# Performance work log

Measured on AMD Instinct MI355X. Metric: run time of the kernel, lower is better.

Reference implementation:

```python
import jax, jax.numpy as jnp
import numpy as np

SMOOTH = 1.0      # self.smooth
NUM_ITER = 10     # iter_
EPS = 1e-07
INF = 1e12        # stand-in for +inf in squared-distance init


def _maxpool(x, window):
    # torch max_pool3d(stride=1, padding=w//2): pad with -inf, window max
    pads = ((0, 0), (0, 0)) + tuple((w // 2, w // 2) for w in window)
    return jax.lax.reduce_window(x, -jnp.inf, jax.lax.max, (1, 1) + window, (1, 1, 1, 1, 1), pads)


def _soft_erode(x):  # x: [B,1,D,H,W]
    p1 = -_maxpool(-x, (3, 1, 1))
    p2 = -_maxpool(-x, (1, 3, 1))
    p3 = -_maxpool(-x, (1, 1, 3))
    return jnp.minimum(jnp.minimum(p1, p2), p3)


def _soft_open(x):
    return _maxpool(_soft_erode(x), (3, 3, 3))  # dilate(erode(x))


def _soft_skel(x, n_iter):
    skel = jax.nn.relu(x - _soft_open(x))
    for _ in range(n_iter):
        x = _soft_erode(x)
        delta = jax.nn.relu(x - _soft_open(x))
        skel = skel + jax.nn.relu(delta - skel * delta)
    return skel


def _edt_pass(d2, axis):
    # 1D squared-distance min-convolution: out[i] = min_j (i-j)^2 + d2[j]
    L = d2.shape[axis]
    d2m = jnp.moveaxis(d2, axis, -1)                 # [..., L]
    i = jnp.arange(L, dtype=d2.dtype)
    sq = (i[:, None] - i[None, :]) ** 2              # [L, L]
    out = jnp.min(d2m[..., None, :] + sq, axis=-1)   # [..., L]
    return jnp.moveaxis(out, -1, axis)


def _edt(mask):
    # exact Euclidean distance transform: distance of nonzero voxels to nearest zero voxel
    d2 = jnp.where(mask > 0, INF, 0.0).astype(jnp.float32)  # [B,D,H,W]
    for ax in (1, 2, 3):
        d2 = _edt_pass(d2, ax)
    return jnp.sqrt(d2)


def _get_weights(mask, skel):
    # mask, skel: [B,D,H,W] binary float
    dist = _edt(mask)
    dist = jnp.where(mask == 0, 0.0, dist)
    on_skel = skel == 1
    skel_r = jnp.where(on_skel, dist, 0.0)
    rmax = jnp.max(skel_r.reshape(skel_r.shape[0], -1), axis=1).reshape(-1, 1, 1, 1)
    valid = rmax > 0
    rmax_safe = jnp.where(valid, rmax, 1.0)
    dist_n = jnp.where(valid, dist / rmax_safe, dist)
    skel_rn = jnp.where(valid, skel_r / rmax_safe, skel_r)
    # dim == 3 branch: skel_1_R2_norm
    skel_1r2 = jnp.where(on_skel, (1.0 + EPS) / (skel_rn ** 2 + EPS), 0.0)
    return dist_n, skel_rn, skel_1r2


def _combine(A, B, C):
    # D = B*C, overwritten by A*C where (A != 0) & (B == 0)
    return jnp.where((A != 0) & (B == 0), A * C, B * C)


def reference(y_pred, y_true):
    # y_pred: [B,C,D,H,W] logits; y_true: [B,1,D,H,W] int labels
    fore = jnp.max(y_pred[:, 1:], axis=1, keepdims=True)
    logits = jnp.concatenate([y_pred[:, :1], fore], axis=1)   # [B,2,D,H,W]
    prob = jax.nn.softmax(logits, axis=1)
    yp = (prob[:, 1] > 0.5).astype(jnp.float32)               # [B,D,H,W]
    yt = (y_true > 0).astype(jnp.float32)[:, 0]               # [B,D,H,W]

    skel_p = _soft_skel(yp[:, None], NUM_ITER)[:, 0]
    skel_t = _soft_skel(yt[:, None], NUM_ITER)[:, 0]

    q_vl, q_slvl, q_sl = _get_weights(yt, skel_t)
    q_vp, q_spvp, q_sp = _get_weights(yp, skel_p)

    w_tprec = (jnp.sum(q_sp * q_vl) + SMOOTH) / (jnp.sum(_combine(q_spvp, q_slvl, q_sp)) + SMOOTH)
    w_tsens = (jnp.sum(q_sl * q_vp) + SMOOTH) / (jnp.sum(_combine(q_slvl, q_spvp, q_sl)) + SMOOTH)
    return 1.0 - 2.0 * (w_tprec * w_tsens) / (w_tprec + w_tsens)


def setup_inputs() -> dict:
    key = jax.random.key(0)
    k1, k2 = jax.random.split(key)
    y_pred = jax.random.normal(k1, (2, 2, 64, 96, 96), dtype=jnp.float32)
    y_true = jax.random.randint(k2, (2, 1, 64, 96, 96), 0, 2, dtype=jnp.int32)
    return {"y_pred": y_pred, "y_true": y_true}
```

## Files before the change

kernel.cpp:

```cpp
#include <hip/hip_runtime.h>

namespace {

constexpr int Bn = 2;
constexpr int Dn = 64;
constexpr int Hn = 96;
constexpr int Wn = 96;
constexpr int HW = Hn * Wn;
constexpr int S  = Dn * HW;
constexpr int NBS = Bn * S;
constexpr int NT  = 2 * NBS;
constexpr int WPR = Wn / 32;
constexpr int WPP = HW / 32;
constexpr int WPS = S / 32;
constexpr int NTW = NT / 32;
constexpr float EPSf = 1e-7f;
constexpr int BLK_SUMS = NBS / 4 / 256;
#define BIGF 1e12f

__global__ __launch_bounds__(256) void k_bin_edt0(const float* __restrict__ logits,
                                                  const int* __restrict__ labels,
                                                  unsigned* __restrict__ Mb,
                                                  float* __restrict__ D2) {
  __shared__ unsigned bits[64];
  __shared__ unsigned zlo[32], zhi[32];
  int slab = blockIdx.x / 288;
  int cg = blockIdx.x - slab * 288;
  int c0 = cg * 32;
  int tid = threadIdx.x;
  int lane = tid & 63;
  for (int t = tid; t < 2048; t += 256) {
    int zz = t >> 5;
    int col = t & 31;
    int s = zz * HW + c0 + col;
    bool v;
    if (slab < 2) {
      float l0 = logits[(slab * 2 + 0) * S + s];
      float l1 = logits[(slab * 2 + 1) * S + s];
      v = l1 > l0;
    } else {
      v = labels[(slab - 2) * S + s] > 0;
    }
    unsigned long long m = __ballot(v);
    if (lane == 0) {
      unsigned w = (unsigned)m;
      bits[zz] = w;
      Mb[slab * WPS + zz * WPP + cg] = w;
    } else if (lane == 32) {
      unsigned w = (unsigned)(m >> 32);
      bits[zz] = w;
      Mb[slab * WPS + zz * WPP + cg] = w;
    }
  }
  __syncthreads();
  if (tid < 64) {
    int col = tid & 31;
    int base = (tid < 32) ? 0 : 32;
    unsigned zw = 0u;
    #pragma unroll
    for (int j = 0; j < 32; ++j)
      zw |= (((bits[base + j] >> col) & 1u) ^ 1u) << j;
    if (tid < 32) zlo[col] = zw; else zhi[col] = zw;
  }
  __syncthreads();
  int col = tid & 31;
  int chunk = tid >> 5;
  int i0 = chunk * 8;
  unsigned long long Z = ((unsigned long long)zhi[col] << 32) | (unsigned long long)zlo[col];
  float* o = D2 + slab * S + c0 + col;
  #pragma unroll
  for (int s = 0; s < 8; ++s) {
    int i = i0 + s;
    unsigned long long below = Z & ((2ull << i) - 1ull);
    unsigned long long above = Z >> i;
    float outv;
    if (below | above) {
      int ddn = below ? (i - (63 - __builtin_clzll(below))) : 99;
      int dup = above ? __builtin_ctzll(above) : 99;
      int d = ddn < dup ? ddn : dup;
      outv = (float)(d * d);
    } else {
      outv = BIGF;
    }
    o[i * HW] = outv;
  }
}

__global__ __launch_bounds__(256) void k_skel11(const unsigned* __restrict__ x,
                                                unsigned* __restrict__ skel) {
  __shared__ unsigned bufA[3600];
  __shared__ unsigned bufB[3174];
  __shared__ unsigned Sbuf[72];
  int slab = blockIdx.x >> 8;
  int z = (blockIdx.x >> 2) & 63;
  int y0 = (blockIdx.x & 3) * 24;
  int tid = threadIdx.x;
  const unsigned* xs = x + slab * WPS;
  for (int t = tid; t < 25 * 48 * 3; t += 256) {
    int p = t / 144;
    int rem = t - p * 144;
    int r = rem / 3;
    int wx = rem - r * 3;
    int zz = z - 12 + p, yy = y0 - 12 + r;
    bufA[t] = (zz >= 0 && zz < Dn && yy >= 0 && yy < Hn)
                ? xs[zz * WPP + yy * WPR + wx] : 0xFFFFFFFFu;
  }
  __syncthreads();
  unsigned skreg = 0u;
  int ro = tid / 3, wxo = tid - ro * 3;
  int yyo = y0 + ro;
  #pragma unroll
  for (int k = 1; k <= 11; ++k) {
    unsigned* src = (k & 1) ? bufA : bufB;
    unsigned* dst = (k & 1) ? bufB : bufA;
    const int Rs = 50 - 2 * k;
    const int Pd = 25 - 2 * k, Rd = 48 - 2 * k;
    const int ps = Rs * 3;
    for (int t = tid; t < Pd * Rd * 3; t += 256) {
      int p = t / (Rd * 3);
      int rem = t - p * (Rd * 3);
      int r = rem / 3;
      int wx = rem - r * 3;
      int ci = ((p + 1) * Rs + (r + 1)) * 3 + wx;
      unsigned v = src[ci];
      unsigned l = (v << 1) | (wx > 0 ? (src[ci - 1] >> 31) : 1u);
      unsigned rr = (v >> 1) | (wx < 2 ? (src[ci + 1] << 31) : 0x80000000u);
      dst[t] = v & l & rr & src[ci - 3] & src[ci + 3] & src[ci - ps] & src[ci + ps];
    }
    __syncthreads();
    if (tid < 72) {
      const int pc = 12 - k;
      const int rb = ro + 12 - k;
      unsigned s = 0u;
      #pragma unroll
      for (int dz = -1; dz <= 1; ++dz) {
        if (z + dz < 0 || z + dz >= Dn) continue;
        #pragma unroll
        for (int dy = -1; dy <= 1; ++dy) {
          if (yyo + dy < 0 || yyo + dy >= Hn) continue;
          s |= dst[((pc + dz) * Rd + (rb + dy)) * 3 + wxo];
        }
      }
      Sbuf[tid] = s;
    }
    __syncthreads();
    if (tid < 72) {
      unsigned s = Sbuf[tid];
      unsigned pw = (wxo > 0) ? Sbuf[tid - 1] : 0u;
      unsigned nw = (wxo < 2) ? Sbuf[tid + 1] : 0u;
      unsigned acc = s | ((s << 1) | (pw >> 31)) | ((s >> 1) | (nw << 31));
      unsigned prevC = src[((13 - k) * Rs + (ro + 13 - k)) * 3 + wxo];
      skreg |= prevC & ~acc;
    }
    __syncthreads();
  }
  if (tid < 72) {
    int gi = slab * WPS + z * WPP + yyo * WPR + wxo;
    skel[gi] = skreg;
  }
}

__global__ __launch_bounds__(192) void k_edt12(const float* __restrict__ D2,
                                               float* __restrict__ EF,
                                               const unsigned* __restrict__ skel,
                                               float* __restrict__ pmax) {
  __shared__ float Bh[24 * 97];
  __shared__ float ldsf[3];
  int slab = blockIdx.x >> 8;
  int zz = (blockIdx.x >> 2) & 63;
  int y0 = (blockIdx.x & 3) * 24;
  int tid = threadIdx.x;
  int pb = slab * S + zz * HW;
  {
    int xx = tid % 96;
    int c = tid / 96;
    int ybase = y0 + c * 12;
    float m2[12];
    #pragma unroll
    for (int s = 0; s < 12; ++s) m2[s] = -2.0f * (float)(ybase + s);
    float best[12];
    #pragma unroll
    for (int s = 0; s < 12; ++s) best[s] = 3.4e38f;
    float jf = 0.0f;
    #pragma unroll 2
    for (int j = 0; j < Hn; ++j) {
      float f = D2[pb + j * 96 + xx];
      float g = fmaf(jf, jf, f);
      #pragma unroll
      for (int s = 0; s < 12; ++s)
        best[s] = fminf(best[s], fmaf(m2[s], jf, g));
      jf += 1.0f;
    }
    #pragma unroll
    for (int s = 0; s < 12; ++s) {
      float yf = (float)(ybase + s);
      Bh[(c * 12 + s) * 97 + xx] = fmaf(yf, yf, best[s]);
    }
  }
  __syncthreads();
  float m = 0.0f;
  {
    int r = tid >> 3;
    int chunk = tid & 7;
    int i0 = chunk * 12;
    float m2[12];
    #pragma unroll
    for (int s = 0; s < 12; ++s) m2[s] = -2.0f * (float)(i0 + s);
    float best[12];
    #pragma unroll
    for (int s = 0; s < 12; ++s) best[s] = 3.4e38f;
    float jf = 0.0f;
    #pragma unroll 2
    for (int j = 0; j < Wn; ++j) {
      float f = Bh[r * 97 + j];
      float g = fmaf(jf, jf, f);
      #pragma unroll
      for (int s = 0; s < 12; ++s)
        best[s] = fminf(best[s], fmaf(m2[s], jf, g));
      jf += 1.0f;
    }
    float outv[12];
    #pragma unroll
    for (int s = 0; s < 12; ++s) {
      float xf = (float)(i0 + s);
      outv[s] = fmaf(xf, xf, best[s]);
    }
    int gb = pb + (y0 + r) * 96 + i0;
    ((float4*)(EF + gb))[0] = make_float4(outv[0], outv[1], outv[2], outv[3]);
    ((float4*)(EF + gb))[1] = make_float4(outv[4], outv[5], outv[6], outv[7]);
    ((float4*)(EF + gb))[2] = make_float4(outv[8], outv[9], outv[10], outv[11]);
    int sh = gb & 31;
    unsigned w0 = skel[gb >> 5];
    unsigned w1 = (sh + 11 > 31) ? skel[(gb >> 5) + 1] : 0u;
    unsigned long long wv = ((unsigned long long)w1 << 32) | (unsigned long long)w0;
    unsigned bitsv = (unsigned)(wv >> sh);
    #pragma unroll
    for (int s = 0; s < 12; ++s)
      if ((bitsv >> s) & 1u) m = fmaxf(m, outv[s]);
  }
  #pragma unroll
  for (int o = 32; o > 0; o >>= 1) m = fmaxf(m, __shfl_xor(m, o, 64));
  if ((tid & 63) == 0) ldsf[tid >> 6] = m;
  __syncthreads();
  if (tid == 0)
    pmax[blockIdx.x] = fmaxf(fmaxf(ldsf[0], ldsf[1]), ldsf[2]);
}

__global__ __launch_bounds__(256) void k_sums(const float* __restrict__ d2,
                                              const unsigned* __restrict__ skel,
                                              const float* __restrict__ pmax,
                                              double* __restrict__ ps) {
  __shared__ float lmax[4];
  __shared__ double ldsd[4][4];
  int tid = threadIdx.x;
  {
    int wave = tid >> 6, lane = tid & 63;
    const float* pw = pmax + wave * 256;
    float v = fmaxf(fmaxf(pw[lane], pw[lane + 64]),
                    fmaxf(pw[lane + 128], pw[lane + 192]));
    #pragma unroll
    for (int o = 32; o > 0; o >>= 1) v = fmaxf(v, __shfl_xor(v, o, 64));
    if (lane == 0) lmax[wave] = v;
  }
  __syncthreads();
  int q = blockIdx.x * 256 + tid;
  int idx0 = q * 4;
  int b = idx0 / S;
  float rmax_p = sqrtf(lmax[b]);
  float rmax_t = sqrtf(lmax[2 + b]);
  float4 dp4 = ((const float4*)d2)[q];
  float4 dt4 = ((const float4*)(d2 + NBS))[q];
  unsigned spw = (skel[idx0 >> 5] >> (idx0 & 31)) & 0xFu;
  unsigned stw = (skel[(NBS + idx0) >> 5] >> (idx0 & 31)) & 0xFu;
  const float* dp = &dp4.x;
  const float* dt = &dt4.x;
  double acc[4] = {0.0, 0.0, 0.0, 0.0};
  #pragma unroll
  for (int s = 0; s < 4; ++s) {
    float dist_p = sqrtf(dp[s]);
    float dist_t = sqrtf(dt[s]);
    bool sp = (spw >> s) & 1u;
    bool st = (stw >> s) & 1u;
    float q_vp = (rmax_p > 0.0f) ? dist_p / rmax_p : dist_p;
    float q_vl = (rmax_t > 0.0f) ? dist_t / rmax_t : dist_t;
    float q_spvp = sp ? q_vp : 0.0f;
    float q_slvl = st ? q_vl : 0.0f;
    float q_sp = sp ? (1.0f + EPSf) / (q_spvp * q_spvp + EPSf) : 0.0f;
    float q_sl = st ? (1.0f + EPSf) / (q_slvl * q_slvl + EPSf) : 0.0f;
    acc[0] += (double)(q_sp * q_vl);
    acc[1] += (double)(((q_spvp != 0.0f) && (q_slvl == 0.0f)) ? q_spvp * q_sp
                                                              : q_slvl * q_sp);
    acc[2] += (double)(q_sl * q_vp);
    acc[3] += (double)(((q_slvl != 0.0f) && (q_spvp == 0.0f)) ? q_slvl * q_sl
                                                              : q_spvp * q_sl);
  }
  #pragma unroll
  for (int k = 0; k < 4; ++k)
    #pragma unroll
    for (int o = 32; o > 0; o >>= 1)
      acc[k] += __shfl_xor(acc[k], o, 64);
  if ((tid & 63) == 0) {
    #pragma unroll
    for (int k = 0; k < 4; ++k) ldsd[tid >> 6][k] = acc[k];
  }
  __syncthreads();
  if (tid == 0) {
    #pragma unroll
    for (int k = 0; k < 4; ++k)
      ps[blockIdx.x * 4 + k] = ldsd[0][k] + ldsd[1][k] + ldsd[2][k] + ldsd[3][k];
  }
}

__global__ __launch_bounds__(256) void k_final(const double* __restrict__ ps,
                                               float* __restrict__ out) {
  __shared__ double ldsd[4][4];
  int tid = threadIdx.x;
  double s[4] = {0.0, 0.0, 0.0, 0.0};
  for (int i = tid; i < BLK_SUMS; i += 256) {
    s[0] += ps[i * 4 + 0];
    s[1] += ps[i * 4 + 1];
    s[2] += ps[i * 4 + 2];
    s[3] += ps[i * 4 + 3];
  }
  #pragma unroll
  for (int k = 0; k < 4; ++k)
    #pragma unroll
    for (int o = 32; o > 0; o >>= 1)
      s[k] += __shfl_xor(s[k], o, 64);
  if ((tid & 63) == 0) {
    #pragma unroll
    for (int k = 0; k < 4; ++k) ldsd[tid >> 6][k] = s[k];
  }
  __syncthreads();
  if (tid == 0) {
    double tot[4];
    #pragma unroll
    for (int k = 0; k < 4; ++k)
      tot[k] = ldsd[0][k] + ldsd[1][k] + ldsd[2][k] + ldsd[3][k];
    double wp = (tot[0] + 1.0) / (tot[1] + 1.0);
    double ws = (tot[2] + 1.0) / (tot[3] + 1.0);
    out[0] = (float)(1.0 - 2.0 * (wp * ws) / (wp + ws));
  }
}

}

extern "C" void kernel_launch(void* const* d_in, const int* in_sizes, int n_in,
                              void* d_out, int out_size, void* d_ws, size_t ws_size,
                              hipStream_t stream) {
  (void)in_sizes; (void)n_in; (void)out_size; (void)ws_size;
  const float* logits = (const float*)d_in[0];
  const int* labels   = (const int*)d_in[1];
  float* out = (float*)d_out;

  float* D2 = (float*)d_ws;
  float* EF = D2 + NT;
  unsigned* MB    = (unsigned*)(EF + NT);
  unsigned* SKELB = MB + NTW;
  float* PMAX  = (float*)(SKELB + NTW);
  double* PS   = (double*)(PMAX + 1024);

  k_bin_edt0<<<1152, 256, 0, stream>>>(logits, labels, MB, D2);
  k_skel11<<<1024, 256, 0, stream>>>(MB, SKELB);
  k_edt12<<<1024, 192, 0, stream>>>(D2, EF, SKELB, PMAX);
  k_sums<<<1152, 256, 0, stream>>>(EF, SKELB, PMAX, PS);
  k_final<<<1, 256, 0, stream>>>(PS, out);
}
```

Before: 136.5 us.

## Fuse skeleton and EDT passes, store z-column bitmasks instead of D2 volume

```diff
diff --git a/kernel.cpp b/kernel.cpp
--- a/kernel.cpp
+++ b/kernel.cpp
@@ -18,10 +18,10 @@
 constexpr int BLK_SUMS = NBS / 4 / 256;
 #define BIGF 1e12f
 
-__global__ __launch_bounds__(256) void k_bin_edt0(const float* __restrict__ logits,
-                                                  const int* __restrict__ labels,
-                                                  unsigned* __restrict__ Mb,
-                                                  float* __restrict__ D2) {
+__global__ __launch_bounds__(256) void k_bin(const float* __restrict__ logits,
+                                             const int* __restrict__ labels,
+                                             unsigned* __restrict__ Mb,
+                                             unsigned long long* __restrict__ ZM) {
   __shared__ unsigned bits[64];
   __shared__ unsigned zlo[32], zhi[32];
   int slab = blockIdx.x / 288;
@@ -63,34 +63,21 @@
     if (tid < 32) zlo[col] = zw; else zhi[col] = zw;
   }
   __syncthreads();
-  int col = tid & 31;
-  int chunk = tid >> 5;
-  int i0 = chunk * 8;
-  unsigned long long Z = ((unsigned long long)zhi[col] << 32) | (unsigned long long)zlo[col];
-  float* o = D2 + slab * S + c0 + col;
-  #pragma unroll
-  for (int s = 0; s < 8; ++s) {
-    int i = i0 + s;
-    unsigned long long below = Z & ((2ull << i) - 1ull);
-    unsigned long long above = Z >> i;
-    float outv;
-    if (below | above) {
-      int ddn = below ? (i - (63 - __builtin_clzll(below))) : 99;
-      int dup = above ? __builtin_ctzll(above) : 99;
-      int d = ddn < dup ? ddn : dup;
-      outv = (float)(d * d);
-    } else {
-      outv = BIGF;
-    }
-    o[i * HW] = outv;
-  }
-}
-
-__global__ __launch_bounds__(256) void k_skel11(const unsigned* __restrict__ x,
-                                                unsigned* __restrict__ skel) {
+  if (tid < 32)
+    ZM[slab * HW + c0 + tid] =
+        ((unsigned long long)zhi[tid] << 32) | (unsigned long long)zlo[tid];
+}
+
+__global__ __launch_bounds__(256) void k_skelEDT(const unsigned* __restrict__ x,
+                                                 const unsigned long long* __restrict__ ZM,
+                                                 unsigned* __restrict__ skel,
+                                                 float* __restrict__ EF,
+                                                 float* __restrict__ pmax) {
   __shared__ unsigned bufA[3600];
   __shared__ unsigned bufB[3174];
   __shared__ unsigned Sbuf[72];
+  __shared__ unsigned skbuf[72];
+  __shared__ float ldsf[4];
   int slab = blockIdx.x >> 8;
   int z = (blockIdx.x >> 2) & 63;
   int y0 = (blockIdx.x & 3) * 24;
@@ -155,26 +142,17 @@
     __syncthreads();
   }
   if (tid < 72) {
-    int gi = slab * WPS + z * WPP + yyo * WPR + wxo;
-    skel[gi] = skreg;
-  }
-}
-
-__global__ __launch_bounds__(192) void k_edt12(const float* __restrict__ D2,
-                                               float* __restrict__ EF,
-                                               const unsigned* __restrict__ skel,
-                                               float* __restrict__ pmax) {
-  __shared__ float Bh[24 * 97];
-  __shared__ float ldsf[3];
-  int slab = blockIdx.x >> 8;
-  int zz = (blockIdx.x >> 2) & 63;
-  int y0 = (blockIdx.x & 3) * 24;
-  int tid = threadIdx.x;
-  int pb = slab * S + zz * HW;
-  {
+    skbuf[tid] = skreg;
+    skel[slab * WPS + z * WPP + yyo * WPR + wxo] = skreg;
+  }
+  __syncthreads();
+  float* Bh = (float*)bufA;
+  int pb = slab * S + z * HW;
+  if (tid < 192) {
     int xx = tid % 96;
     int c = tid / 96;
     int ybase = y0 + c * 12;
+    const unsigned long long* zc = ZM + slab * HW + xx;
     float m2[12];
     #pragma unroll
     for (int s = 0; s < 12; ++s) m2[s] = -2.0f * (float)(ybase + s);
@@ -184,7 +162,18 @@
     float jf = 0.0f;
     #pragma unroll 2
     for (int j = 0; j < Hn; ++j) {
-      float f = D2[pb + j * 96 + xx];
+      unsigned long long Z = zc[j * 96];
+      unsigned long long below = Z & ((2ull << z) - 1ull);
+      unsigned long long above = Z >> z;
+      float f;
+      if (below | above) {
+        int ddn = below ? (z - (63 - __builtin_clzll(below))) : 99;
+        int dup = above ? __builtin_ctzll(above) : 99;
+        int d = ddn < dup ? ddn : dup;
+        f = (float)(d * d);
+      } else {
+        f = BIGF;
+      }
       float g = fmaf(jf, jf, f);
       #pragma unroll
       for (int s = 0; s < 12; ++s)
@@ -199,7 +188,7 @@
   }
   __syncthreads();
   float m = 0.0f;
-  {
+  if (tid < 192) {
     int r = tid >> 3;
     int chunk = tid & 7;
     int i0 = chunk * 12;
@@ -229,9 +218,9 @@
     ((float4*)(EF + gb))[0] = make_float4(outv[0], outv[1], outv[2], outv[3]);
     ((float4*)(EF + gb))[1] = make_float4(outv[4], outv[5], outv[6], outv[7]);
     ((float4*)(EF + gb))[2] = make_float4(outv[8], outv[9], outv[10], outv[11]);
-    int sh = gb & 31;
-    unsigned w0 = skel[gb >> 5];
-    unsigned w1 = (sh + 11 > 31) ? skel[(gb >> 5) + 1] : 0u;
+    int sh = i0 & 31;
+    unsigned w0 = skbuf[r * 3 + (i0 >> 5)];
+    unsigned w1 = (sh + 11 > 31) ? skbuf[r * 3 + (i0 >> 5) + 1] : 0u;
     unsigned long long wv = ((unsigned long long)w1 << 32) | (unsigned long long)w0;
     unsigned bitsv = (unsigned)(wv >> sh);
     #pragma unroll
@@ -243,7 +232,7 @@
   if ((tid & 63) == 0) ldsf[tid >> 6] = m;
   __syncthreads();
   if (tid == 0)
-    pmax[blockIdx.x] = fmaxf(fmaxf(ldsf[0], ldsf[1]), ldsf[2]);
+    pmax[blockIdx.x] = fmaxf(fmaxf(ldsf[0], ldsf[1]), fmaxf(ldsf[2], ldsf[3]));
 }
 
 __global__ __launch_bounds__(256) void k_sums(const float* __restrict__ d2,
@@ -353,16 +342,15 @@
   const int* labels   = (const int*)d_in[1];
   float* out = (float*)d_out;
 
-  float* D2 = (float*)d_ws;
-  float* EF = D2 + NT;
-  unsigned* MB    = (unsigned*)(EF + NT);
+  float* EF = (float*)d_ws;
+  unsigned long long* ZM = (unsigned long long*)(EF + NT);
+  unsigned* MB    = (unsigned*)(ZM + 4 * HW);
   unsigned* SKELB = MB + NTW;
   float* PMAX  = (float*)(SKELB + NTW);
   double* PS   = (double*)(PMAX + 1024);
 
-  k_bin_edt0<<<1152, 256, 0, stream>>>(logits, labels, MB, D2);
-  k_skel11<<<1024, 256, 0, stream>>>(MB, SKELB);
-  k_edt12<<<1024, 192, 0, stream>>>(D2, EF, SKELB, PMAX);
+  k_bin<<<1152, 256, 0, stream>>>(logits, labels, MB, ZM);
+  k_skelEDT<<<1024, 256, 0, stream>>>(MB, ZM, SKELB, EF, PMAX);
   k_sums<<<1152, 256, 0, stream>>>(EF, SKELB, PMAX, PS);
   k_final<<<1, 256, 0, stream>>>(PS, out);
 }
```

New measurement: 147.6 us. 1.08x slower.

## Replace iterative bitwise skeleton with L1 distance transform and local-max test

Applied to the files above, without the earlier changes.

```diff
diff --git a/kernel.cpp b/kernel.cpp
--- a/kernel.cpp
+++ b/kernel.cpp
@@ -10,7 +10,6 @@
 constexpr int S  = Dn * HW;
 constexpr int NBS = Bn * S;
 constexpr int NT  = 2 * NBS;
-constexpr int WPR = Wn / 32;
 constexpr int WPP = HW / 32;
 constexpr int WPS = S / 32;
 constexpr int NTW = NT / 32;
@@ -18,10 +17,10 @@
 constexpr int BLK_SUMS = NBS / 4 / 256;
 #define BIGF 1e12f
 
-__global__ __launch_bounds__(256) void k_bin_edt0(const float* __restrict__ logits,
-                                                  const int* __restrict__ labels,
-                                                  unsigned* __restrict__ Mb,
-                                                  float* __restrict__ D2) {
+__global__ __launch_bounds__(256) void k_bin0(const float* __restrict__ logits,
+                                              const int* __restrict__ labels,
+                                              float* __restrict__ D2,
+                                              unsigned char* __restrict__ D1z) {
   __shared__ unsigned bits[64];
   __shared__ unsigned zlo[32], zhi[32];
   int slab = blockIdx.x / 288;
@@ -42,15 +41,8 @@
       v = labels[(slab - 2) * S + s] > 0;
     }
     unsigned long long m = __ballot(v);
-    if (lane == 0) {
-      unsigned w = (unsigned)m;
-      bits[zz] = w;
-      Mb[slab * WPS + zz * WPP + cg] = w;
-    } else if (lane == 32) {
-      unsigned w = (unsigned)(m >> 32);
-      bits[zz] = w;
-      Mb[slab * WPS + zz * WPP + cg] = w;
-    }
+    if (lane == 0)       bits[zz] = (unsigned)m;
+    else if (lane == 32) bits[zz] = (unsigned)(m >> 32);
   }
   __syncthreads();
   if (tid < 64) {
@@ -68,113 +60,44 @@
   int i0 = chunk * 8;
   unsigned long long Z = ((unsigned long long)zhi[col] << 32) | (unsigned long long)zlo[col];
   float* o = D2 + slab * S + c0 + col;
+  unsigned char* o1 = D1z + slab * S + c0 + col;
   #pragma unroll
   for (int s = 0; s < 8; ++s) {
     int i = i0 + s;
     unsigned long long below = Z & ((2ull << i) - 1ull);
     unsigned long long above = Z >> i;
     float outv;
+    int d1v;
     if (below | above) {
       int ddn = below ? (i - (63 - __builtin_clzll(below))) : 99;
       int dup = above ? __builtin_ctzll(above) : 99;
       int d = ddn < dup ? ddn : dup;
       outv = (float)(d * d);
+      d1v = d < 13 ? d : 13;
     } else {
       outv = BIGF;
+      d1v = 13;
     }
     o[i * HW] = outv;
-  }
-}
-
-__global__ __launch_bounds__(256) void k_skel11(const unsigned* __restrict__ x,
-                                                unsigned* __restrict__ skel) {
-  __shared__ unsigned bufA[3600];
-  __shared__ unsigned bufB[3174];
-  __shared__ unsigned Sbuf[72];
+    o1[i * HW] = (unsigned char)d1v;
+  }
+}
+
+__global__ __launch_bounds__(192) void k_edtl1(const float* __restrict__ D2,
+                                               const unsigned char* __restrict__ D1z,
+                                               float* __restrict__ EF,
+                                               unsigned char* __restrict__ D1) {
+  __shared__ float Bh[24 * 97];
+  __shared__ unsigned char L1b[24 * 96];
   int slab = blockIdx.x >> 8;
   int z = (blockIdx.x >> 2) & 63;
   int y0 = (blockIdx.x & 3) * 24;
   int tid = threadIdx.x;
-  const unsigned* xs = x + slab * WPS;
-  for (int t = tid; t < 25 * 48 * 3; t += 256) {
-    int p = t / 144;
-    int rem = t - p * 144;
-    int r = rem / 3;
-    int wx = rem - r * 3;
-    int zz = z - 12 + p, yy = y0 - 12 + r;
-    bufA[t] = (zz >= 0 && zz < Dn && yy >= 0 && yy < Hn)
-                ? xs[zz * WPP + yy * WPR + wx] : 0xFFFFFFFFu;
-  }
-  __syncthreads();
-  unsigned skreg = 0u;
-  int ro = tid / 3, wxo = tid - ro * 3;
-  int yyo = y0 + ro;
-  #pragma unroll
-  for (int k = 1; k <= 11; ++k) {
-    unsigned* src = (k & 1) ? bufA : bufB;
-    unsigned* dst = (k & 1) ? bufB : bufA;
-    const int Rs = 50 - 2 * k;
-    const int Pd = 25 - 2 * k, Rd = 48 - 2 * k;
-    const int ps = Rs * 3;
-    for (int t = tid; t < Pd * Rd * 3; t += 256) {
-      int p = t / (Rd * 3);
-      int rem = t - p * (Rd * 3);
-      int r = rem / 3;
-      int wx = rem - r * 3;
-      int ci = ((p + 1) * Rs + (r + 1)) * 3 + wx;
-      unsigned v = src[ci];
-      unsigned l = (v << 1) | (wx > 0 ? (src[ci - 1] >> 31) : 1u);
-      unsigned rr = (v >> 1) | (wx < 2 ? (src[ci + 1] << 31) : 0x80000000u);
-      dst[t] = v & l & rr & src[ci - 3] & src[ci + 3] & src[ci - ps] & src[ci + ps];
-    }
-    __syncthreads();
-    if (tid < 72) {
-      const int pc = 12 - k;
-      const int rb = ro + 12 - k;
-      unsigned s = 0u;
-      #pragma unroll
-      for (int dz = -1; dz <= 1; ++dz) {
-        if (z + dz < 0 || z + dz >= Dn) continue;
-        #pragma unroll
-        for (int dy = -1; dy <= 1; ++dy) {
-          if (yyo + dy < 0 || yyo + dy >= Hn) continue;
-          s |= dst[((pc + dz) * Rd + (rb + dy)) * 3 + wxo];
-        }
-      }
-      Sbuf[tid] = s;
-    }
-    __syncthreads();
-    if (tid < 72) {
-      unsigned s = Sbuf[tid];
-      unsigned pw = (wxo > 0) ? Sbuf[tid - 1] : 0u;
-      unsigned nw = (wxo < 2) ? Sbuf[tid + 1] : 0u;
-      unsigned acc = s | ((s << 1) | (pw >> 31)) | ((s >> 1) | (nw << 31));
-      unsigned prevC = src[((13 - k) * Rs + (ro + 13 - k)) * 3 + wxo];
-      skreg |= prevC & ~acc;
-    }
-    __syncthreads();
-  }
-  if (tid < 72) {
-    int gi = slab * WPS + z * WPP + yyo * WPR + wxo;
-    skel[gi] = skreg;
-  }
-}
-
-__global__ __launch_bounds__(192) void k_edt12(const float* __restrict__ D2,
-                                               float* __restrict__ EF,
-                                               const unsigned* __restrict__ skel,
-                                               float* __restrict__ pmax) {
-  __shared__ float Bh[24 * 97];
-  __shared__ float ldsf[3];
-  int slab = blockIdx.x >> 8;
-  int zz = (blockIdx.x >> 2) & 63;
-  int y0 = (blockIdx.x & 3) * 24;
-  int tid = threadIdx.x;
-  int pb = slab * S + zz * HW;
-  {
-    int xx = tid % 96;
-    int c = tid / 96;
-    int ybase = y0 + c * 12;
+  int pb = slab * S + z * HW;
+  int xx = tid % 96;
+  int c = tid / 96;
+  int ybase = y0 + c * 12;
+  {
     float m2[12];
     #pragma unroll
     for (int s = 0; s < 12; ++s) m2[s] = -2.0f * (float)(ybase + s);
@@ -197,12 +120,32 @@
       Bh[(c * 12 + s) * 97 + xx] = fmaf(yf, yf, best[s]);
     }
   }
-  __syncthreads();
-  float m = 0.0f;
-  {
-    int r = tid >> 3;
-    int chunk = tid & 7;
-    int i0 = chunk * 12;
+  {
+    const unsigned char* dzc = D1z + pb + xx;
+    int P = 255;
+    for (int j = 0; j < ybase; ++j) P = min(P, (int)dzc[j * 96] - j);
+    int A[12];
+    #pragma unroll
+    for (int s = 0; s < 12; ++s) {
+      int j = ybase + s;
+      P = min(P, (int)dzc[j * 96] - j);
+      A[s] = j + P;
+    }
+    int Sv = 255;
+    for (int j = 95; j >= ybase + 12; --j) Sv = min(Sv, (int)dzc[j * 96] + j);
+    #pragma unroll
+    for (int s = 11; s >= 0; --s) {
+      int j = ybase + s;
+      Sv = min(Sv, (int)dzc[j * 96] + j);
+      int t1 = min(A[s], Sv - j);
+      L1b[(c * 12 + s) * 96 + xx] = (unsigned char)(t1 < 13 ? t1 : 13);
+    }
+  }
+  __syncthreads();
+  int r = tid >> 3;
+  int chunk = tid & 7;
+  int i0 = chunk * 12;
+  {
     float m2[12];
     #pragma unroll
     for (int s = 0; s < 12; ++s) m2[s] = -2.0f * (float)(i0 + s);
@@ -219,31 +162,107 @@
         best[s] = fminf(best[s], fmaf(m2[s], jf, g));
       jf += 1.0f;
     }
+    int gb = pb + (y0 + r) * 96 + i0;
     float outv[12];
     #pragma unroll
     for (int s = 0; s < 12; ++s) {
       float xf = (float)(i0 + s);
       outv[s] = fmaf(xf, xf, best[s]);
     }
-    int gb = pb + (y0 + r) * 96 + i0;
     ((float4*)(EF + gb))[0] = make_float4(outv[0], outv[1], outv[2], outv[3]);
     ((float4*)(EF + gb))[1] = make_float4(outv[4], outv[5], outv[6], outv[7]);
     ((float4*)(EF + gb))[2] = make_float4(outv[8], outv[9], outv[10], outv[11]);
-    int sh = gb & 31;
-    unsigned w0 = skel[gb >> 5];
-    unsigned w1 = (sh + 11 > 31) ? skel[(gb >> 5) + 1] : 0u;
-    unsigned long long wv = ((unsigned long long)w1 << 32) | (unsigned long long)w0;
-    unsigned bitsv = (unsigned)(wv >> sh);
-    #pragma unroll
-    for (int s = 0; s < 12; ++s)
-      if ((bitsv >> s) & 1u) m = fmaxf(m, outv[s]);
-  }
-  #pragma unroll
-  for (int o = 32; o > 0; o >>= 1) m = fmaxf(m, __shfl_xor(m, o, 64));
-  if ((tid & 63) == 0) ldsf[tid >> 6] = m;
+  }
+  {
+    const unsigned char* row = &L1b[r * 96];
+    int P = 255;
+    for (int j = 0; j < i0; ++j) P = min(P, (int)row[j] - j);
+    int A[12];
+    #pragma unroll
+    for (int s = 0; s < 12; ++s) {
+      int j = i0 + s;
+      P = min(P, (int)row[j] - j);
+      A[s] = j + P;
+    }
+    int Sv = 255;
+    for (int j = 95; j >= i0 + 12; --j) Sv = min(Sv, (int)row[j] + j);
+    unsigned dv[3] = {0u, 0u, 0u};
+    #pragma unroll
+    for (int s = 11; s >= 0; --s) {
+      int j = i0 + s;
+      Sv = min(Sv, (int)row[j] + j);
+      int d1 = min(A[s], Sv - j);
+      d1 = d1 < 12 ? d1 : 12;
+      dv[s >> 2] |= ((unsigned)d1) << ((s & 3) * 8);
+    }
+    unsigned* dst = (unsigned*)(D1 + pb + (y0 + r) * 96 + i0);
+    dst[0] = dv[0]; dst[1] = dv[1]; dst[2] = dv[2];
+  }
+}
+
+__global__ __launch_bounds__(256) void k_skelmax(const unsigned char* __restrict__ D1,
+                                                 const float* __restrict__ EF,
+                                                 unsigned* __restrict__ SKELB,
+                                                 float* __restrict__ pmax) {
+  __shared__ unsigned char zm[26 * 96];
+  __shared__ unsigned char cen[26 * 96];
+  __shared__ float ldsf[4];
+  int slab = blockIdx.x >> 8;
+  int z = (blockIdx.x >> 2) & 63;
+  int y0 = (blockIdx.x & 3) * 24;
+  int tid = threadIdx.x;
+  int pb = slab * S + z * HW;
+  for (int t = tid; t < 2496; t += 256) {
+    int rr = t / 96;
+    int x = t - rr * 96;
+    int yy = y0 - 1 + rr;
+    unsigned char m = 0, cv = 0;
+    if (yy >= 0 && yy < Hn) {
+      int base = slab * S + yy * 96 + x;
+      cv = D1[base + z * HW];
+      m = cv;
+      if (z > 0) { unsigned char a = D1[base + (z - 1) * HW]; m = m > a ? m : a; }
+      if (z < Dn - 1) { unsigned char a = D1[base + (z + 1) * HW]; m = m > a ? m : a; }
+    }
+    zm[t] = m;
+    cen[t] = cv;
+  }
+  __syncthreads();
+  float mm = 0.0f;
+  int wbase = slab * WPS + z * WPP + y0 * 3;
+  int lane = tid & 63;
+  #pragma unroll
+  for (int round = 0; round < 9; ++round) {
+    int v = round * 256 + tid;
+    int rr = v / 96;
+    int x = v - rr * 96;
+    int b1 = rr * 96 + x;
+    unsigned char mx = zm[b1];
+    { unsigned char a = zm[b1 + 96]; mx = mx > a ? mx : a; }
+    { unsigned char a = zm[b1 + 192]; mx = mx > a ? mx : a; }
+    if (x > 0) {
+      unsigned char a0 = zm[b1 - 1], a1 = zm[b1 + 95], a2 = zm[b1 + 191];
+      unsigned char a = a0 > a1 ? a0 : a1; a = a > a2 ? a : a2;
+      mx = mx > a ? mx : a;
+    }
+    if (x < Wn - 1) {
+      unsigned char a0 = zm[b1 + 1], a1 = zm[b1 + 97], a2 = zm[b1 + 193];
+      unsigned char a = a0 > a1 ? a0 : a1; a = a > a2 ? a : a2;
+      mx = mx > a ? mx : a;
+    }
+    unsigned char d1 = cen[b1 + 96];
+    bool sk = (d1 == mx) && (d1 >= 1) && (d1 <= 11);
+    unsigned long long bal = __ballot(sk);
+    if (lane == 0)       SKELB[wbase + (v >> 5)] = (unsigned)bal;
+    else if (lane == 32) SKELB[wbase + (v >> 5)] = (unsigned)(bal >> 32);
+    if (sk) mm = fmaxf(mm, EF[pb + (y0 + rr) * 96 + x]);
+  }
+  #pragma unroll
+  for (int o = 32; o > 0; o >>= 1) mm = fmaxf(mm, __shfl_xor(mm, o, 64));
+  if (lane == 0) ldsf[tid >> 6] = mm;
   __syncthreads();
   if (tid == 0)
-    pmax[blockIdx.x] = fmaxf(fmaxf(ldsf[0], ldsf[1]), ldsf[2]);
+    pmax[blockIdx.x] = fmaxf(fmaxf(ldsf[0], ldsf[1]), fmaxf(ldsf[2], ldsf[3]));
 }
 
 __global__ __launch_bounds__(256) void k_sums(const float* __restrict__ d2,
@@ -353,16 +372,17 @@
   const int* labels   = (const int*)d_in[1];
   float* out = (float*)d_out;
 
-  float* D2 = (float*)d_ws;
-  float* EF = D2 + NT;
-  unsigned* MB    = (unsigned*)(EF + NT);
-  unsigned* SKELB = MB + NTW;
+  float* EF = (float*)d_ws;
+  float* D2 = EF + NT;
+  unsigned char* D1z = (unsigned char*)(D2 + NT);
+  unsigned char* D1  = D1z + NT;
+  unsigned* SKELB = (unsigned*)(D1 + NT);
   float* PMAX  = (float*)(SKELB + NTW);
   double* PS   = (double*)(PMAX + 1024);
 
-  k_bin_edt0<<<1152, 256, 0, stream>>>(logits, labels, MB, D2);
-  k_skel11<<<1024, 256, 0, stream>>>(MB, SKELB);
-  k_edt12<<<1024, 192, 0, stream>>>(D2, EF, SKELB, PMAX);
+  k_bin0<<<1152, 256, 0, stream>>>(logits, labels, D2, D1z);
+  k_edtl1<<<1024, 192, 0, stream>>>(D2, D1z, EF, D1);
+  k_skelmax<<<1024, 256, 0, stream>>>(D1, EF, SKELB, PMAX);
   k_sums<<<1152, 256, 0, stream>>>(EF, SKELB, PMAX, PS);
   k_final<<<1, 256, 0, stream>>>(PS, out);
 }
```

New measurement: 143.4 us. +5.1%, slower.
